# Performance work log

Measured on AMD Instinct MI355X. Metric: run time of the kernel, lower is better.

Reference implementation:

```python
import jax, jax.numpy as jnp
import numpy as np

D_MODEL = 4096
D_HIDDEN = 32768
BATCH = 2048
K = 128
N_DEAD = 2048


def _ln(x, eps=1e-5):
    # torch .std() is unbiased (ddof=1)
    mu = jnp.mean(x, axis=-1, keepdims=True)
    xc = x - mu
    std = jnp.std(x, axis=-1, keepdims=True, ddof=1)
    return xc / (std + eps), mu, std


def _topk_activation(x, k):
    # topk over last dim, relu values, scatter back into zeros
    vals, idx = jax.lax.top_k(x, k)          # [B, k]
    vals = jax.nn.relu(vals)
    rows = jnp.arange(x.shape[0])[:, None]    # [B, 1]
    return jnp.zeros_like(x).at[rows, idx].set(vals)


def setup_inputs() -> dict:
    key = jax.random.key(0)
    k1, k2 = jax.random.split(key)
    x = jax.random.normal(k1, (BATCH, D_MODEL), dtype=jnp.float32)
    # kaiming-uniform-ish encoder init
    bound = 1.0 / np.sqrt(D_MODEL)
    w_enc = jax.random.uniform(k2, (D_MODEL, D_HIDDEN), dtype=jnp.float32,
                               minval=-bound, maxval=bound)
    w_dec = w_enc.T
    w_dec = w_dec / jnp.linalg.norm(w_dec, axis=0, keepdims=True)
    b_enc = jnp.zeros((D_HIDDEN,), dtype=jnp.float32)
    b_pre = jnp.zeros((D_MODEL,), dtype=jnp.float32)
    # fixed dead-neuron mask with exactly N_DEAD dead latents
    dm = np.zeros((D_HIDDEN,), dtype=bool)
    rng = np.random.default_rng(0)
    dm[rng.choice(D_HIDDEN, size=N_DEAD, replace=False)] = True
    dead_mask = jnp.asarray(dm)
    return {"x": x, "w_enc": w_enc, "w_dec": w_dec, "b_enc": b_enc,
            "b_pre": b_pre, "dead_mask": dead_mask, "num_dead": N_DEAD}


def reference(x, w_enc, w_dec, b_enc, b_pre, dead_mask, num_dead):
    xn, mu, std = _ln(x)
    xc = xn - b_pre
    pre_acts = xc @ w_enc + b_enc                 # [B, d_hidden]
    latents = _topk_activation(pre_acts, K)
    recons = latents @ w_dec + b_pre              # [B, d_model]
    recons = recons * std + mu
    # auxk dead-neuron path (num_dead is a static python int)
    k_aux = min(x.shape[-1] // 2, num_dead)
    auxk_latents = jnp.where(dead_mask[None, :], pre_acts, -jnp.inf)
    auxk_acts = _topk_activation(auxk_latents, k_aux)
    auxk = auxk_acts @ w_dec + b_pre
    auxk = auxk * std + mu
    return recons, auxk, num_dead
```

## Files before the change

### kernel.cpp

```cpp
#include <hip/hip_runtime.h>
#include <math.h>

#define D_MODEL  4096
#define D_HIDDEN 32768
#define BATCH    2048
#define KSEL     128
#define NDEAD    2048
#define TIECAP   256

typedef short s16x8 __attribute__((ext_vector_type(8)));
typedef float f32x4 __attribute__((ext_vector_type(4)));

__device__ __forceinline__ unsigned int fkey(float f) {
    unsigned int u = __float_as_uint(f);
    return (u & 0x80000000u) ? ~u : (u | 0x80000000u);
}
__device__ __forceinline__ unsigned short f2bf(float f) {
    unsigned int u = __float_as_uint(f);
    u += 0x7FFFu + ((u >> 16) & 1u);
    return (unsigned short)(u >> 16);
}
__device__ __forceinline__ float bf2f(unsigned short h) {
    return __uint_as_float(((unsigned int)h) << 16);
}
__device__ __forceinline__ unsigned int key16x2(unsigned int u) {
    const unsigned int s = (u >> 15) & 0x10001u;
    const unsigned int mask = s * 0xFFFFu;
    return (u ^ mask) | (~mask & 0x80008000u);
}
__device__ __forceinline__ float unkey16(unsigned int k) {
    const unsigned int u = (k & 0x8000u) ? (k & 0x7FFFu) : (~k & 0xFFFFu);
    return __uint_as_float(u << 16);
}
__device__ __forceinline__ void async_copy16(void* lds_dst, const void* gsrc) {
    __builtin_amdgcn_global_load_lds(
        (const __attribute__((address_space(1))) unsigned int*)gsrc,
        (__attribute__((address_space(3))) unsigned int*)lds_dst,
        16, 0, 0);
}

__global__ __launch_bounds__(256) void prep_kernel(
    const float* __restrict__ x, const float* __restrict__ b_pre,
    double* __restrict__ mu, double* __restrict__ stdv, double* __restrict__ sinv,
    unsigned short* __restrict__ Ahp, float* __restrict__ xch, float* __restrict__ xcl)
{
    const int row = blockIdx.x;
    const int tid = threadIdx.x;
    const float* xr = x + (size_t)row * D_MODEL;
    float xv[16];
#pragma unroll
    for (int i = 0; i < 16; ++i) xv[i] = xr[tid + 256 * i];
    double s = 0.0;
#pragma unroll
    for (int i = 0; i < 16; ++i) s += (double)xv[i];
    __shared__ double red[4];
    __shared__ double sh_mu, sh_si;
    const int lane = tid & 63, wid = tid >> 6;
#pragma unroll
    for (int off = 32; off > 0; off >>= 1) s += __shfl_down(s, off, 64);
    if (lane == 0) red[wid] = s;
    __syncthreads();
    if (tid == 0) sh_mu = (red[0] + red[1] + red[2] + red[3]) / (double)D_MODEL;
    __syncthreads();
    const double m = sh_mu;
    double s2 = 0.0;
#pragma unroll
    for (int i = 0; i < 16; ++i) { double d = (double)xv[i] - m; s2 += d * d; }
#pragma unroll
    for (int off = 32; off > 0; off >>= 1) s2 += __shfl_down(s2, off, 64);
    __syncthreads();
    if (lane == 0) red[wid] = s2;
    __syncthreads();
    if (tid == 0) {
        double var = (red[0] + red[1] + red[2] + red[3]) / (double)(D_MODEL - 1);
        double sd = sqrt(var);
        mu[row] = m;
        stdv[row] = sd;
        const double si = 1.0 / (sd + 1e-5);
        sinv[row] = si;
        sh_si = si;
    }
    __syncthreads();
    const double si = sh_si;
#pragma unroll
    for (int i = 0; i < 4; ++i) {
        const int j = (i * 256 + tid) * 4;
        const float4 x4 = *(const float4*)(xr + j);
        const float4 bp = *(const float4*)(b_pre + j);
        float vf[4], hi[4], lo[4];
        const float xe[4] = {x4.x, x4.y, x4.z, x4.w};
        const float be[4] = {bp.x, bp.y, bp.z, bp.w};
#pragma unroll
        for (int e = 0; e < 4; ++e) {
            const double t = ((double)xe[e] - m) * si;
            vf[e] = (float)t - be[e];
            const double a = t - (double)be[e];
            hi[e] = (float)a;
            lo[e] = (float)(a - (double)hi[e]);
        }
        uint2 hw;
        hw.x = (unsigned)f2bf(vf[0]) | ((unsigned)f2bf(vf[1]) << 16);
        hw.y = (unsigned)f2bf(vf[2]) | ((unsigned)f2bf(vf[3]) << 16);
        *(uint2*)(Ahp + (size_t)row * D_MODEL + j) = hw;
        *(float4*)(xch + (size_t)row * D_MODEL + j) = make_float4(hi[0], hi[1], hi[2], hi[3]);
        *(float4*)(xcl + (size_t)row * D_MODEL + j) = make_float4(lo[0], lo[1], lo[2], lo[3]);
    }
}

__global__ void dead_scan_kernel(const unsigned char* __restrict__ mask8,
                                 int* __restrict__ dead_idx, int* __restrict__ dead_cnt,
                                 const int* __restrict__ num_dead_in, float* __restrict__ out_last)
{
    const int lane = threadIdx.x;
    int c = 0;
    for (int j = lane; j < D_HIDDEN; j += 64) c += (mask8[j] != 0);
#pragma unroll
    for (int off = 32; off > 0; off >>= 1) c += __shfl_down(c, off, 64);
    const int total_u8 = __shfl(c, 0, 64);
    const bool u8mode = (total_u8 == NDEAD);
    const int* mask32 = (const int*)mask8;
    int cnt = 0;
    for (int base = 0; base < D_HIDDEN; base += 64) {
        const int j = base + lane;
        const bool d = u8mode ? (mask8[j] != 0) : (mask32[j] != 0);
        const unsigned long long b = __ballot(d);
        const int pre = __popcll(b & ((1ull << lane) - 1ull));
        if (d && (cnt + pre) < NDEAD) dead_idx[cnt + pre] = j;
        cnt += __popcll(b);
    }
    const int cc = cnt > NDEAD ? NDEAD : cnt;
    if (lane == 0) {
        *dead_cnt = cc;
        *out_last = (float)(*num_dead_in);
    }
    for (int t = cc + lane; t < NDEAD; t += 64) dead_idx[t] = 0;
}

__global__ __launch_bounds__(256) void bsplit_kernel(
    const float* __restrict__ w_enc, unsigned short* __restrict__ Bhp)
{
    __shared__ float t[32][33];
    const int bk = blockIdx.x * 32;
    const int bn = blockIdx.y * 32;
    const int tid = threadIdx.x;
    const int lr = tid >> 3, lc4 = (tid & 7) * 4;
    const float4 v = *(const float4*)(w_enc + (size_t)(bk + lr) * D_HIDDEN + bn + lc4);
    t[lr][lc4 + 0] = v.x; t[lr][lc4 + 1] = v.y; t[lr][lc4 + 2] = v.z; t[lr][lc4 + 3] = v.w;
    __syncthreads();
    float o[4];
#pragma unroll
    for (int j = 0; j < 4; ++j) o[j] = t[lc4 + j][lr];
    uint2 hw;
    hw.x = (unsigned)f2bf(o[0]) | ((unsigned)f2bf(o[1]) << 16);
    hw.y = (unsigned)f2bf(o[2]) | ((unsigned)f2bf(o[3]) << 16);
    *(uint2*)(Bhp + (size_t)(bn + lr) * D_MODEL + bk + lc4) = hw;
}

__global__ __launch_bounds__(256) void wencT_kernel(
    const float* __restrict__ w_enc, float* __restrict__ wT)
{
    __shared__ float t[32][33];
    const int bk = blockIdx.x * 32;
    const int bn = blockIdx.y * 32;
    const int tid = threadIdx.x;
    const int lr = tid >> 3, lc4 = (tid & 7) * 4;
    const float4 v = *(const float4*)(w_enc + (size_t)(bk + lr) * D_HIDDEN + bn + lc4);
    t[lr][lc4 + 0] = v.x; t[lr][lc4 + 1] = v.y; t[lr][lc4 + 2] = v.z; t[lr][lc4 + 3] = v.w;
    __syncthreads();
    const int j = tid >> 3, i4 = (tid & 7) * 4;
    float4 o;
    o.x = t[i4 + 0][j]; o.y = t[i4 + 1][j]; o.z = t[i4 + 2][j]; o.w = t[i4 + 3][j];
    *(float4*)(wT + (size_t)(bn + j) * D_MODEL + bk + i4) = o;
}

__global__ __launch_bounds__(256) void wprep_kernel(
    const float* __restrict__ w_enc, unsigned short* __restrict__ Bhp,
    float* __restrict__ wT)
{
    __shared__ float t[32][33];
    const int bk = blockIdx.x * 32;
    const int bn = blockIdx.y * 32;
    const int tid = threadIdx.x;
    const int lr = tid >> 3, lc4 = (tid & 7) * 4;
    const float4 v = *(const float4*)(w_enc + (size_t)(bk + lr) * D_HIDDEN + bn + lc4);
    t[lr][lc4 + 0] = v.x; t[lr][lc4 + 1] = v.y; t[lr][lc4 + 2] = v.z; t[lr][lc4 + 3] = v.w;
    __syncthreads();
    float o[4];
#pragma unroll
    for (int j = 0; j < 4; ++j) o[j] = t[lc4 + j][lr];
    uint2 hw;
    hw.x = (unsigned)f2bf(o[0]) | ((unsigned)f2bf(o[1]) << 16);
    hw.y = (unsigned)f2bf(o[2]) | ((unsigned)f2bf(o[3]) << 16);
    *(uint2*)(Bhp + (size_t)(bn + lr) * D_MODEL + bk + lc4) = hw;
    *(float4*)(wT + (size_t)(bn + lr) * D_MODEL + bk + lc4) = make_float4(o[0], o[1], o[2], o[3]);
}

template<int EPI>
__global__ __launch_bounds__(512) void mm256_kernel(
    const unsigned short* __restrict__ A, const unsigned short* __restrict__ B,
    const int kdim, const int ntiles_x,
    const float* __restrict__ bias_n,
    const double* __restrict__ muv, const double* __restrict__ stdvv,
    void* __restrict__ outp, const long ostride)
{
    __shared__ unsigned short lds[2 * 4 * 8192];
    const int tid = threadIdx.x;
    const int lane = tid & 63, wid = tid >> 6;
    const int cpx = gridDim.x >> 3;
    const int orig = blockIdx.x;
    const int wg = (orig & 7) * cpx + (orig >> 3);
    const int m0 = (wg % ntiles_x) * 256;
    const int n0 = (wg / ntiles_x) * 256;
    const int wm = (wid >> 2) * 128;
    const int wn = (wid & 3) * 64;
    const int fr = lane & 15, kq = lane >> 4;
    const int swr = (fr >> 1) & 3;
    const int qg = (lane & 3) ^ ((lane >> 3) & 3);
    const int qo = (kq ^ swr) * 8;

    f32x4 acc[8][4];
#pragma unroll
    for (int i = 0; i < 8; ++i)
#pragma unroll
        for (int j = 0; j < 4; ++j) acc[i][j] = (f32x4){0.f, 0.f, 0.f, 0.f};

    const unsigned short* sH0[4];
    int dH0[4];
#pragma unroll
    for (int j = 0; j < 4; ++j) {
        const int g = wid * 4 + j;
        const int is_b = g >> 4;
        const int sr = g & 15;
        const unsigned short* gp = is_b ? B : A;
        const int t0 = is_b ? n0 : m0;
        sH0[j] = gp + (size_t)(t0 + sr * 16 + (lane >> 2)) * kdim + qg * 8;
        dH0[j] = (is_b ? 2 : 0) * 8192 + sr * 512;
    }

    const int NT = kdim >> 6;
#pragma unroll
    for (int j = 0; j < 4; ++j) async_copy16(lds + dH0[j], sH0[j]);
#pragma unroll
    for (int j = 0; j < 4; ++j) async_copy16(lds + 8192 + dH0[j], sH0[j] + 32);
    if (NT > 1) {
#pragma unroll
        for (int j = 0; j < 4; ++j) async_copy16(lds + 32768 + dH0[j], sH0[j] + 64);
    }

    for (int t = 0; t < NT; ++t) {
        const int cur = t & 1;
        unsigned short* bb = (unsigned short*)lds + cur * 32768;
        unsigned short* nb = (unsigned short*)lds + (cur ^ 1) * 32768;
        const int k1 = (t + 1) << 6;
        const int k2 = (t + 2) << 6;

        if (t < NT - 1) { asm volatile("s_waitcnt vmcnt(8)" ::: "memory"); }
        else            { asm volatile("s_waitcnt vmcnt(4)" ::: "memory"); }
        asm volatile("s_barrier" ::: "memory");
        __builtin_amdgcn_sched_barrier(0);
        {
            if (t + 1 < NT) {
                async_copy16(nb + 8192 + dH0[0], sH0[0] + k1 + 32);
                async_copy16(nb + 8192 + dH0[1], sH0[1] + k1 + 32);
            }
            s16x8 a[4], b[4];
#pragma unroll
            for (int mi = 0; mi < 4; ++mi)
                a[mi] = *(const s16x8*)(bb + (wm + mi * 16 + fr) * 32 + qo);
#pragma unroll
            for (int ni = 0; ni < 4; ++ni)
                b[ni] = *(const s16x8*)(bb + 2 * 8192 + (wn + ni * 16 + fr) * 32 + qo);
            __builtin_amdgcn_s_setprio(1);
#pragma unroll
            for (int mi = 0; mi < 4; ++mi)
#pragma unroll
                for (int ni = 0; ni < 4; ++ni)
                    acc[mi][ni] = __builtin_amdgcn_mfma_f32_16x16x32_bf16(a[mi], b[ni], acc[mi][ni], 0, 0, 0);
            __builtin_amdgcn_s_setprio(0);
            asm volatile("s_barrier" ::: "memory");
            __builtin_amdgcn_sched_barrier(0);
            if (t + 1 < NT) {
                async_copy16(nb + 8192 + dH0[2], sH0[2] + k1 + 32);
                async_copy16(nb + 8192 + dH0[3], sH0[3] + k1 + 32);
            }
            s16x8 a2[4];
#pragma unroll
            for (int mi = 0; mi < 4; ++mi)
                a2[mi] = *(const s16x8*)(bb + (wm + (mi + 4) * 16 + fr) * 32 + qo);
            __builtin_amdgcn_s_setprio(1);
#pragma unroll
            for (int mi = 0; mi < 4; ++mi)
#pragma unroll
                for (int ni = 0; ni < 4; ++ni)
                    acc[mi + 4][ni] = __builtin_amdgcn_mfma_f32_16x16x32_bf16(a2[mi], b[ni], acc[mi + 4][ni], 0, 0, 0);
            __builtin_amdgcn_s_setprio(0);
        }
        if (t < NT - 1) { asm volatile("s_waitcnt vmcnt(8)" ::: "memory"); }
        else            { asm volatile("s_waitcnt vmcnt(0)" ::: "memory"); }
        asm volatile("s_barrier" ::: "memory");
        __builtin_amdgcn_sched_barrier(0);
        {
            if (t + 2 < NT) {
                async_copy16(bb + dH0[0], sH0[0] + k2);
                async_copy16(bb + dH0[1], sH0[1] + k2);
            }
            s16x8 a[4], b[4];
#pragma unroll
            for (int mi = 0; mi < 4; ++mi)
                a[mi] = *(const s16x8*)(bb + 8192 + (wm + mi * 16 + fr) * 32 + qo);
#pragma unroll
            for (int ni = 0; ni < 4; ++ni)
                b[ni] = *(const s16x8*)(bb + 3 * 8192 + (wn + ni * 16 + fr) * 32 + qo);
            __builtin_amdgcn_s_setprio(1);
#pragma unroll
            for (int mi = 0; mi < 4; ++mi)
#pragma unroll
                for (int ni = 0; ni < 4; ++ni)
                    acc[mi][ni] = __builtin_amdgcn_mfma_f32_16x16x32_bf16(a[mi], b[ni], acc[mi][ni], 0, 0, 0);
            __builtin_amdgcn_s_setprio(0);
            asm volatile("s_barrier" ::: "memory");
            __builtin_amdgcn_sched_barrier(0);
            if (t + 2 < NT) {
                async_copy16(bb + dH0[2], sH0[2] + k2);
                async_copy16(bb + dH0[3], sH0[3] + k2);
            }
            s16x8 a2[4];
#pragma unroll
            for (int mi = 0; mi < 4; ++mi)
                a2[mi] = *(const s16x8*)(bb + 8192 + (wm + (mi + 4) * 16 + fr) * 32 + qo);
            __builtin_amdgcn_s_setprio(1);
#pragma unroll
            for (int mi = 0; mi < 4; ++mi)
#pragma unroll
                for (int ni = 0; ni < 4; ++ni)
                    acc[mi + 4][ni] = __builtin_amdgcn_mfma_f32_16x16x32_bf16(a2[mi], b[ni], acc[mi + 4][ni], 0, 0, 0);
            __builtin_amdgcn_s_setprio(0);
        }
    }

#pragma unroll
    for (int ni = 0; ni < 4; ++ni) {
        const int col = n0 + wn + ni * 16 + fr;
        const float be = bias_n[col];
#pragma unroll
        for (int mi = 0; mi < 8; ++mi) {
            const int rb = m0 + wm + mi * 16 + kq * 4;
            if (EPI == 0) {
                unsigned short* O = (unsigned short*)outp;
#pragma unroll
                for (int r = 0; r < 4; ++r)
                    O[(size_t)(rb + r) * ostride + col] = f2bf(acc[mi][ni][r] + be);
            } else {
                float* O = (float*)outp;
#pragma unroll
                for (int r = 0; r < 4; ++r) {
                    const int m = rb + r;
                    O[(size_t)m * ostride + col] =
                        (acc[mi][ni][r] + be) * (float)stdvv[m] + (float)muv[m];
                }
            }
        }
    }
}

template<int EPI>
__global__ __launch_bounds__(256) void mm_kernel(
    const unsigned short* __restrict__ A, const unsigned short* __restrict__ B,
    const int kdim, const int ntiles_x,
    const float* __restrict__ bias_n,
    const double* __restrict__ muv, const double* __restrict__ stdvv,
    void* __restrict__ outp, const long ostride)
{
    __shared__ unsigned short lds[3 * 2 * 128 * 32];
    const int tid = threadIdx.x;
    const int lane = tid & 63, wid = tid >> 6;
    const int cpx = gridDim.x >> 3;
    const int orig = blockIdx.x;
    const int wg = (orig & 7) * cpx + (orig >> 3);
    const int m0 = (wg % ntiles_x) * 128;
    const int n0 = (wg / ntiles_x) * 128;
    const int wm = (wid >> 1) * 64, wn = (wid & 1) * 64;
    const int fr = lane & 15, kq = lane >> 4;
    const int swr = (fr >> 1) & 3;
    const int qg = (lane & 3) ^ ((lane >> 3) & 3);
    const int qo = (kq ^ swr) * 8;

    f32x4 acc[4][4];
#pragma unroll
    for (int i = 0; i < 4; ++i)
#pragma unroll
        for (int j = 0; j < 4; ++j) acc[i][j] = (f32x4){0.f, 0.f, 0.f, 0.f};

    const unsigned short* srcs[4];
    int d0[4];
#pragma unroll
    for (int j = 0; j < 4; ++j) {
        const int s = wid * 4 + j;
        const int pl = s >> 3, sr = s & 7;
        const int r = sr * 16 + (lane >> 2);
        srcs[j] = (pl ? B : A) + (size_t)((pl ? n0 : m0) + r) * kdim + qg * 8;
        d0[j] = pl * 4096 + sr * 512;
    }

    const int NT = kdim >> 5;
#pragma unroll
    for (int j = 0; j < 4; ++j) async_copy16(lds + 0 * 8192 + d0[j], srcs[j]);
#pragma unroll
    for (int j = 0; j < 4; ++j) async_copy16(lds + 1 * 8192 + d0[j], srcs[j] + 32);

    int cur = 0, nxt = 2;
    for (int t = 0; t < NT; ++t) {
        if (t < NT - 1) {
            asm volatile("s_waitcnt vmcnt(4)" ::: "memory");
        } else {
            asm volatile("s_waitcnt vmcnt(0)" ::: "memory");
        }
        __builtin_amdgcn_s_barrier();
        __builtin_amdgcn_sched_barrier(0);

        if (t + 2 < NT) {
            const int k2 = (t + 2) << 5;
#pragma unroll
            for (int j = 0; j < 4; ++j) async_copy16(lds + nxt * 8192 + d0[j], srcs[j] + k2);
        }

        const unsigned short* la = lds + cur * 8192;
        const unsigned short* lb = la + 4096;
        s16x8 a[4], b[4];
#pragma unroll
        for (int i = 0; i < 4; ++i) {
            a[i] = *(const s16x8*)(la + (wm + i * 16 + fr) * 32 + qo);
            b[i] = *(const s16x8*)(lb + (wn + i * 16 + fr) * 32 + qo);
        }
#pragma unroll
        for (int mi = 0; mi < 4; ++mi)
#pragma unroll
            for (int ni = 0; ni < 4; ++ni)
                acc[mi][ni] = __builtin_amdgcn_mfma_f32_16x16x32_bf16(a[mi], b[ni], acc[mi][ni], 0, 0, 0);

        cur = cur == 2 ? 0 : cur + 1;
        nxt = nxt == 2 ? 0 : nxt + 1;
    }

#pragma unroll
    for (int ni = 0; ni < 4; ++ni) {
        const int col = n0 + wn + ni * 16 + fr;
        const float be = bias_n[col];
#pragma unroll
        for (int mi = 0; mi < 4; ++mi) {
            const int rb = m0 + wm + mi * 16 + kq * 4;
            if (EPI == 0) {
                unsigned short* O = (unsigned short*)outp;
#pragma unroll
                for (int r = 0; r < 4; ++r)
                    O[(size_t)(rb + r) * ostride + col] = f2bf(acc[mi][ni][r] + be);
            } else {
                float* O = (float*)outp;
#pragma unroll
                for (int r = 0; r < 4; ++r) {
                    const int m = rb + r;
                    O[(size_t)m * ostride + col] =
                        (acc[mi][ni][r] + be) * (float)stdvv[m] + (float)muv[m];
                }
            }
        }
    }
}

__global__ __launch_bounds__(256) void topk_sel_kernel(
    const unsigned short* __restrict__ p16,
    int* __restrict__ topk_idx, float* __restrict__ topk_val,
    int* __restrict__ sure_cnt, int* __restrict__ tie_cnt, int* __restrict__ cand_col)
{
    const int row = blockIdx.x;
    const int tid = threadIdx.x;
    const int lane = tid & 63, wid = tid >> 6;
    const unsigned short* pr = p16 + (size_t)row * D_HIDDEN;

    __shared__ int red[4];
    __shared__ int sh_sel, sh_tie;

    uint4 kr[16];
#pragma unroll
    for (int i = 0; i < 16; ++i) {
        uint4 w = *(const uint4*)(pr + (i * 256 + tid) * 8);
        w.x = key16x2(w.x); w.y = key16x2(w.y); w.z = key16x2(w.z); w.w = key16x2(w.w);
        kr[i] = w;
    }
    if (tid == 0) { sh_sel = 0; sh_tie = 0; }

    unsigned int lo = 0, hi = 65535;
    while (lo < hi) {
        const unsigned int mid = (lo + hi) >> 1;
        int c = 0;
#pragma unroll
        for (int i = 0; i < 16; ++i) {
            const unsigned int u[4] = {kr[i].x, kr[i].y, kr[i].z, kr[i].w};
#pragma unroll
            for (int e = 0; e < 4; ++e) {
                c += (int)((u[e] & 0xFFFFu) > mid);
                c += (int)((u[e] >> 16) > mid);
            }
        }
#pragma unroll
        for (int off = 32; off > 0; off >>= 1) c += __shfl_down(c, off, 64);
        if (lane == 0) red[wid] = c;
        __syncthreads();
        const int total = red[0] + red[1] + red[2] + red[3];
        if (total < KSEL) hi = mid; else lo = mid + 1;
        __syncthreads();
    }
    const unsigned int K16 = lo;

    const float vc = unkey16(K16);
    const float DLT = 1.3e-2f;
    const float sureT = vc + 2.f * DLT;
    const float candT = vc - 2.f * DLT;
    const unsigned int sK = fkey(sureT) >> 16;
    const unsigned int cK = fkey(candT) >> 16;

    int* oidx = topk_idx + row * KSEL;
    float* oval = topk_val + row * KSEL;
    int* cc = cand_col + row * TIECAP;
#pragma unroll
    for (int i = 0; i < 16; ++i) {
        const int j0 = (i * 256 + tid) * 8;
        const unsigned int u[4] = {kr[i].x, kr[i].y, kr[i].z, kr[i].w};
#pragma unroll
        for (int e = 0; e < 8; ++e) {
            const unsigned int k = (e & 1) ? (u[e >> 1] >> 16) : (u[e >> 1] & 0xFFFFu);
            if (k < cK) continue;
            const float v = unkey16(k);
            if (k > sK && v > sureT) {
                const int pos = atomicAdd(&sh_sel, 1);
                oidx[pos] = j0 + e;
                oval[pos] = v > 0.f ? v : 0.f;
            } else if (v >= candT) {
                const int t = atomicAdd(&sh_tie, 1);
                if (t < TIECAP) cc[t] = j0 + e;
            }
        }
    }
    __syncthreads();
    if (tid == 0) {
        sure_cnt[row] = sh_sel;
        tie_cnt[row] = sh_tie > TIECAP ? TIECAP : sh_tie;
    }
}

__global__ __launch_bounds__(256) void topk_refine_kernel(
    const int* __restrict__ tie_cnt, const int* __restrict__ cand_col,
    double* __restrict__ cand_val,
    const float* __restrict__ xch, const float* __restrict__ xcl,
    const float* __restrict__ wT, const float* __restrict__ b_enc)
{
    const int row = blockIdx.x;
    const int tid = threadIdx.x;
    const int lane = tid & 63, wid = tid >> 6;
    const int T = tie_cnt[row];
    const int base = (int)blockIdx.y * 4 + wid;
    if (base >= T) return;
    const float* hr = xch + (size_t)row * D_MODEL;
    const float* lr2 = xcl + (size_t)row * D_MODEL;
    for (int slot = base; slot < T; slot += 64) {
        const int col = cand_col[row * TIECAP + slot];
        const float* wr = wT + (size_t)col * D_MODEL;
        double s0 = 0.0, s1 = 0.0;
        for (int k = lane * 4; k < D_MODEL; k += 512) {
            {
                const float4 h = *(const float4*)(hr + k);
                const float4 l = *(const float4*)(lr2 + k);
                const float4 w4 = *(const float4*)(wr + k);
                s0 += ((double)h.x + (double)l.x) * (double)w4.x;
                s0 += ((double)h.y + (double)l.y) * (double)w4.y;
                s0 += ((double)h.z + (double)l.z) * (double)w4.z;
                s0 += ((double)h.w + (double)l.w) * (double)w4.w;
            }
            {
                const int k2 = k + 256;
                const float4 h = *(const float4*)(hr + k2);
                const float4 l = *(const float4*)(lr2 + k2);
                const float4 w4 = *(const float4*)(wr + k2);
                s1 += ((double)h.x + (double)l.x) * (double)w4.x;
                s1 += ((double)h.y + (double)l.y) * (double)w4.y;
                s1 += ((double)h.z + (double)l.z) * (double)w4.z;
                s1 += ((double)h.w + (double)l.w) * (double)w4.w;
            }
        }
        double s = s0 + s1;
#pragma unroll
        for (int off = 32; off > 0; off >>= 1) s += __shfl_down(s, off, 64);
        if (lane == 0) cand_val[row * TIECAP + slot] = s + (double)b_enc[col];
    }
}

__global__ __launch_bounds__(256) void topk_fin_kernel(
    const int* __restrict__ sure_cnt, const int* __restrict__ tie_cnt,
    const int* __restrict__ cand_col, const double* __restrict__ cand_val,
    int* __restrict__ topk_idx, float* __restrict__ topk_val)
{
    const int row = blockIdx.x;
    const int tid = threadIdx.x;
    __shared__ double vals[TIECAP];
    __shared__ int cols[TIECAP];
    const int G = sure_cnt[row];
    const int T = tie_cnt[row];
    const int R = KSEL - G;
    if (tid < T) {
        vals[tid] = cand_val[row * TIECAP + tid];
        cols[tid] = cand_col[row * TIECAP + tid];
    }
    __syncthreads();
    int* oidx = topk_idx + row * KSEL;
    float* oval = topk_val + row * KSEL;
    if (tid < T) {
        const double v = vals[tid];
        const int c = cols[tid];
        int rank = 0;
        for (int u = 0; u < T; ++u) {
            const double vu = vals[u];
            rank += (int)((vu > v) || (vu == v && cols[u] < c));
        }
        if (rank < R) {
            oidx[G + rank] = c;
            oval[G + rank] = v > 0.0 ? (float)v : 0.f;
        }
    }
    const int take = R < T ? R : T;
    if (tid >= take && tid < R) {
        oidx[G + tid] = (T > 0) ? cols[0] : 0;
        oval[G + tid] = 0.f;
    }
}

__global__ __launch_bounds__(256) void wdec2bf_kernel(
    const float* __restrict__ w_dec, unsigned short* __restrict__ wd16)
{
    const size_t gid = (size_t)blockIdx.x * 256 + threadIdx.x;
    const size_t base = gid * 8;
    const float4 a = *(const float4*)(w_dec + base);
    const float4 b = *(const float4*)(w_dec + base + 4);
    uint4 o;
    o.x = (unsigned)f2bf(a.x) | ((unsigned)f2bf(a.y) << 16);
    o.y = (unsigned)f2bf(a.z) | ((unsigned)f2bf(a.w) << 16);
    o.z = (unsigned)f2bf(b.x) | ((unsigned)f2bf(b.y) << 16);
    o.w = (unsigned)f2bf(b.z) | ((unsigned)f2bf(b.w) << 16);
    *(uint4*)(wd16 + base) = o;
}

__global__ __launch_bounds__(256) void decode_kernel(
    const int* __restrict__ topk_idx, const float* __restrict__ topk_val,
    const unsigned short* __restrict__ wd16, const float* __restrict__ b_pre,
    const double* __restrict__ mu, const double* __restrict__ stdv,
    float* __restrict__ out0)
{
    const int row = blockIdx.x;
    const int tid = threadIdx.x;
    __shared__ int sidx[KSEL];
    __shared__ float sval[KSEL];
    if (tid < KSEL) {
        sidx[tid] = topk_idx[row * KSEL + tid];
        sval[tid] = topk_val[row * KSEL + tid];
    }
    __syncthreads();
    float acc[16];
#pragma unroll
    for (int i = 0; i < 16; ++i) acc[i] = 0.f;
    const int dbase = tid * 16;
    for (int k = 0; k < KSEL; ++k) {
        const float v = sval[k];
        if (v == 0.f) continue;
        const uint4* wr = (const uint4*)(wd16 + (size_t)sidx[k] * D_MODEL + dbase);
        const uint4 w0 = wr[0], w1 = wr[1];
        const unsigned int u[8] = {w0.x, w0.y, w0.z, w0.w, w1.x, w1.y, w1.z, w1.w};
#pragma unroll
        for (int i = 0; i < 8; ++i) {
            acc[2 * i]     += v * __uint_as_float(u[i] << 16);
            acc[2 * i + 1] += v * __uint_as_float(u[i] & 0xFFFF0000u);
        }
    }
    const float st = (float)stdv[row];
    const float mm = (float)mu[row];
    float* o = out0 + (size_t)row * D_MODEL + dbase;
#pragma unroll
    for (int i = 0; i < 16; ++i) {
        o[i] = (acc[i] + b_pre[dbase + i]) * st + mm;
    }
}

__global__ __launch_bounds__(256) void auxg_kernel(
    const unsigned short* __restrict__ p16, const int* __restrict__ dead_idx,
    const int* __restrict__ dead_cnt, unsigned short* __restrict__ Ahd)
{
    const int r = blockIdx.x;
    const int tid = threadIdx.x;
    const int dc = *dead_cnt;
#pragma unroll
    for (int i = 0; i < 8; ++i) {
        const int c = i * 256 + tid;
        unsigned short v = 0;
        if (c < dc) {
            const unsigned short u = p16[(size_t)r * D_HIDDEN + dead_idx[c]];
            v = (u & 0x8000u) ? (unsigned short)0 : u;
        }
        Ahd[(size_t)r * NDEAD + c] = v;
    }
}

__global__ __launch_bounds__(256) void auxb_kernel(
    const float* __restrict__ w_dec, const int* __restrict__ dead_idx,
    unsigned short* __restrict__ Bhd)
{
    __shared__ float t[32][33];
    const int k0 = blockIdx.x * 32;
    const int n0 = blockIdx.y * 32;
    const int tid = threadIdx.x;
    const int i = tid >> 3, j4 = (tid & 7) * 4;
    const int srow = dead_idx[k0 + i];
    const float4 v = *(const float4*)(w_dec + (size_t)srow * D_MODEL + n0 + j4);
    t[i][j4 + 0] = v.x; t[i][j4 + 1] = v.y; t[i][j4 + 2] = v.z; t[i][j4 + 3] = v.w;
    __syncthreads();
    const int j = tid >> 3, i4 = (tid & 7) * 4;
    uint2 hw;
    hw.x = (unsigned)f2bf(t[i4 + 0][j]) | ((unsigned)f2bf(t[i4 + 1][j]) << 16);
    hw.y = (unsigned)f2bf(t[i4 + 2][j]) | ((unsigned)f2bf(t[i4 + 3][j]) << 16);
    *(uint2*)(Bhd + (size_t)(n0 + j) * NDEAD + k0 + i4) = hw;
}

extern "C" void kernel_launch(void* const* d_in, const int* in_sizes, int n_in,
                              void* d_out, int out_size, void* d_ws, size_t ws_size,
                              hipStream_t stream)
{
    (void)in_sizes; (void)n_in; (void)out_size;
    const float* x      = (const float*)d_in[0];
    const float* w_enc  = (const float*)d_in[1];
    const float* w_dec  = (const float*)d_in[2];
    const float* b_enc  = (const float*)d_in[3];
    const float* b_pre  = (const float*)d_in[4];
    const unsigned char* dead_mask = (const unsigned char*)d_in[5];
    const int* num_dead = (const int*)d_in[6];
    float* out = (float*)d_out;

    char* base = (char*)d_ws;
    char* w = base;
    auto alloc = [&](size_t bytes) -> char* {
        char* p = w;
        w += (bytes + 255) & ~(size_t)255;
        return p;
    };
    unsigned short* p16 = (unsigned short*)alloc((size_t)BATCH * D_HIDDEN * 2);
    double* mu       = (double*)alloc((size_t)BATCH * 8);
    double* stdv     = (double*)alloc((size_t)BATCH * 8);
    double* sinv     = (double*)alloc((size_t)BATCH * 8);
    int* topk_idx    = (int*)alloc((size_t)BATCH * KSEL * 4);
    float* topk_val  = (float*)alloc((size_t)BATCH * KSEL * 4);
    int* dead_idx    = (int*)alloc((size_t)NDEAD * 4);
    int* dead_cnt    = (int*)alloc(256);
    int* sure_cnt    = (int*)alloc((size_t)BATCH * 4);
    int* tie_cnt     = (int*)alloc((size_t)BATCH * 4);
    int* cand_col    = (int*)alloc((size_t)BATCH * TIECAP * 4);
    double* cand_val = (double*)alloc((size_t)BATCH * TIECAP * 8);
    float* xch       = (float*)alloc((size_t)BATCH * D_MODEL * 4);
    float* xcl       = (float*)alloc((size_t)BATCH * D_MODEL * 4);
    unsigned short* Ahp = (unsigned short*)alloc((size_t)BATCH * D_MODEL * 2);
    char* region     = alloc((size_t)D_HIDDEN * D_MODEL * 4);
    const size_t need_small = (size_t)(w - base);
    float* wT_big    = (float*)alloc((size_t)D_HIDDEN * D_MODEL * 4);
    const size_t need_big = (size_t)(w - base);
    const bool bigws = (ws_size >= need_big);
    (void)need_small;

    unsigned short* Bhp = (unsigned short*)region;
    float* wT_small = (float*)region;
    unsigned short* wd16 = (unsigned short*)region;
    unsigned short* Bhd  = (unsigned short*)(region + (size_t)D_HIDDEN * D_MODEL * 2);
    unsigned short* Ahd  = Ahp;
    float* wT = bigws ? wT_big : wT_small;

    float* out0 = out;
    float* out1 = out + (size_t)BATCH * D_MODEL;
    float* out_last = out + (size_t)2 * BATCH * D_MODEL;

    prep_kernel<<<BATCH, 256, 0, stream>>>(x, b_pre, mu, stdv, sinv, Ahp, xch, xcl);
    dead_scan_kernel<<<1, 64, 0, stream>>>(dead_mask, dead_idx, dead_cnt, num_dead, out_last);
    if (bigws) {
        wprep_kernel<<<dim3(D_MODEL / 32, D_HIDDEN / 32), 256, 0, stream>>>(w_enc, Bhp, wT);
    } else {
        bsplit_kernel<<<dim3(D_MODEL / 32, D_HIDDEN / 32), 256, 0, stream>>>(w_enc, Bhp);
    }
    mm256_kernel<0><<<(BATCH / 256) * (D_HIDDEN / 256), 512, 0, stream>>>(
        Ahp, Bhp, D_MODEL, BATCH / 256, b_enc, nullptr, nullptr, p16, (long)D_HIDDEN);
    if (!bigws) {
        wencT_kernel<<<dim3(D_MODEL / 32, D_HIDDEN / 32), 256, 0, stream>>>(w_enc, wT);
    }
    topk_sel_kernel<<<BATCH, 256, 0, stream>>>(p16, topk_idx, topk_val, sure_cnt, tie_cnt, cand_col);
    topk_refine_kernel<<<dim3(BATCH, 16), 256, 0, stream>>>(
        tie_cnt, cand_col, cand_val, xch, xcl, wT, b_enc);
    topk_fin_kernel<<<BATCH, 256, 0, stream>>>(
        sure_cnt, tie_cnt, cand_col, cand_val, topk_idx, topk_val);
    auxg_kernel<<<BATCH, 256, 0, stream>>>(p16, dead_idx, dead_cnt, Ahd);
    auxb_kernel<<<dim3(NDEAD / 32, D_MODEL / 32), 256, 0, stream>>>(w_dec, dead_idx, Bhd);
    wdec2bf_kernel<<<(int)(((size_t)D_HIDDEN * D_MODEL) / (256 * 8)), 256, 0, stream>>>(w_dec, wd16);
    decode_kernel<<<BATCH, 256, 0, stream>>>(topk_idx, topk_val, wd16, b_pre, mu, stdv, out0);
    mm_kernel<1><<<(BATCH / 128) * (D_MODEL / 128), 256, 0, stream>>>(
        Ahd, Bhd, NDEAD, BATCH / 128, b_pre, mu, stdv, out1, (long)D_MODEL);
}
```

Before: 2.123 ms.

## Merge small kernels into combined launches and reuse 256-tile GEMM for aux path

Folds the dead-mask scan into an extra block of the prep kernel, and merges top-k selection, aux gather, aux weight transpose and decoder bf16 conversion into one block-partitioned kernel. It also merges top-k finalization into the decode kernel, keeping the selected indices in shared memory. The aux GEMM now uses the 256-tile mm256 kernel instead of the 128-tile one. This cuts launch count and lets independent work share the GPU at once, at the cost of a heterogeneous grid whose blocks differ in register and LDS use.

```diff
diff --git a/kernel.cpp b/kernel.cpp
--- a/kernel.cpp
+++ b/kernel.cpp
@@ -8,6 +8,11 @@
 #define NDEAD    2048
 #define TIECAP   256
 
+#define NB_SEL 2048
+#define NB_AG  2048
+#define NB_AB  8192
+#define NB_WD  8192
+
 typedef short s16x8 __attribute__((ext_vector_type(8)));
 typedef float f32x4 __attribute__((ext_vector_type(4)));
 
@@ -42,10 +47,40 @@
 __global__ __launch_bounds__(256) void prep_kernel(
     const float* __restrict__ x, const float* __restrict__ b_pre,
     double* __restrict__ mu, double* __restrict__ stdv, double* __restrict__ sinv,
-    unsigned short* __restrict__ Ahp, float* __restrict__ xch, float* __restrict__ xcl)
+    unsigned short* __restrict__ Ahp, float* __restrict__ xch, float* __restrict__ xcl,
+    const unsigned char* __restrict__ mask8, int* __restrict__ dead_idx,
+    int* __restrict__ dead_cnt, const int* __restrict__ num_dead_in,
+    float* __restrict__ out_last)
 {
     const int row = blockIdx.x;
     const int tid = threadIdx.x;
+    if (row == BATCH) {
+        if (tid >= 64) return;
+        const int lane = tid;
+        int c = 0;
+        for (int j = lane; j < D_HIDDEN; j += 64) c += (mask8[j] != 0);
+#pragma unroll
+        for (int off = 32; off > 0; off >>= 1) c += __shfl_down(c, off, 64);
+        const int total_u8 = __shfl(c, 0, 64);
+        const bool u8mode = (total_u8 == NDEAD);
+        const int* mask32 = (const int*)mask8;
+        int cnt = 0;
+        for (int base = 0; base < D_HIDDEN; base += 64) {
+            const int j = base + lane;
+            const bool d = u8mode ? (mask8[j] != 0) : (mask32[j] != 0);
+            const unsigned long long b = __ballot(d);
+            const int pre = __popcll(b & ((1ull << lane) - 1ull));
+            if (d && (cnt + pre) < NDEAD) dead_idx[cnt + pre] = j;
+            cnt += __popcll(b);
+        }
+        const int cc = cnt > NDEAD ? NDEAD : cnt;
+        if (lane == 0) {
+            *dead_cnt = cc;
+            *out_last = (float)(*num_dead_in);
+        }
+        for (int t = cc + lane; t < NDEAD; t += 64) dead_idx[t] = 0;
+        return;
+    }
     const float* xr = x + (size_t)row * D_MODEL;
     float xv[16];
 #pragma unroll
@@ -105,35 +140,6 @@
         *(float4*)(xch + (size_t)row * D_MODEL + j) = make_float4(hi[0], hi[1], hi[2], hi[3]);
         *(float4*)(xcl + (size_t)row * D_MODEL + j) = make_float4(lo[0], lo[1], lo[2], lo[3]);
     }
-}
-
-__global__ void dead_scan_kernel(const unsigned char* __restrict__ mask8,
-                                 int* __restrict__ dead_idx, int* __restrict__ dead_cnt,
-                                 const int* __restrict__ num_dead_in, float* __restrict__ out_last)
-{
-    const int lane = threadIdx.x;
-    int c = 0;
-    for (int j = lane; j < D_HIDDEN; j += 64) c += (mask8[j] != 0);
-#pragma unroll
-    for (int off = 32; off > 0; off >>= 1) c += __shfl_down(c, off, 64);
-    const int total_u8 = __shfl(c, 0, 64);
-    const bool u8mode = (total_u8 == NDEAD);
-    const int* mask32 = (const int*)mask8;
-    int cnt = 0;
-    for (int base = 0; base < D_HIDDEN; base += 64) {
-        const int j = base + lane;
-        const bool d = u8mode ? (mask8[j] != 0) : (mask32[j] != 0);
-        const unsigned long long b = __ballot(d);
-        const int pre = __popcll(b & ((1ull << lane) - 1ull));
-        if (d && (cnt + pre) < NDEAD) dead_idx[cnt + pre] = j;
-        cnt += __popcll(b);
-    }
-    const int cc = cnt > NDEAD ? NDEAD : cnt;
-    if (lane == 0) {
-        *dead_cnt = cc;
-        *out_last = (float)(*num_dead_in);
-    }
-    for (int t = cc + lane; t < NDEAD; t += 64) dead_idx[t] = 0;
 }
 
 __global__ __launch_bounds__(256) void bsplit_kernel(
@@ -363,189 +369,175 @@
     }
 }
 
-template<int EPI>
-__global__ __launch_bounds__(256) void mm_kernel(
-    const unsigned short* __restrict__ A, const unsigned short* __restrict__ B,
-    const int kdim, const int ntiles_x,
-    const float* __restrict__ bias_n,
-    const double* __restrict__ muv, const double* __restrict__ stdvv,
-    void* __restrict__ outp, const long ostride)
-{
-    __shared__ unsigned short lds[3 * 2 * 128 * 32];
-    const int tid = threadIdx.x;
-    const int lane = tid & 63, wid = tid >> 6;
-    const int cpx = gridDim.x >> 3;
-    const int orig = blockIdx.x;
-    const int wg = (orig & 7) * cpx + (orig >> 3);
-    const int m0 = (wg % ntiles_x) * 128;
-    const int n0 = (wg / ntiles_x) * 128;
-    const int wm = (wid >> 1) * 64, wn = (wid & 1) * 64;
-    const int fr = lane & 15, kq = lane >> 4;
-    const int swr = (fr >> 1) & 3;
-    const int qg = (lane & 3) ^ ((lane >> 3) & 3);
-    const int qo = (kq ^ swr) * 8;
-
-    f32x4 acc[4][4];
-#pragma unroll
-    for (int i = 0; i < 4; ++i)
-#pragma unroll
-        for (int j = 0; j < 4; ++j) acc[i][j] = (f32x4){0.f, 0.f, 0.f, 0.f};
-
-    const unsigned short* srcs[4];
-    int d0[4];
-#pragma unroll
-    for (int j = 0; j < 4; ++j) {
-        const int s = wid * 4 + j;
-        const int pl = s >> 3, sr = s & 7;
-        const int r = sr * 16 + (lane >> 2);
-        srcs[j] = (pl ? B : A) + (size_t)((pl ? n0 : m0) + r) * kdim + qg * 8;
-        d0[j] = pl * 4096 + sr * 512;
-    }
-
-    const int NT = kdim >> 5;
-#pragma unroll
-    for (int j = 0; j < 4; ++j) async_copy16(lds + 0 * 8192 + d0[j], srcs[j]);
-#pragma unroll
-    for (int j = 0; j < 4; ++j) async_copy16(lds + 1 * 8192 + d0[j], srcs[j] + 32);
-
-    int cur = 0, nxt = 2;
-    for (int t = 0; t < NT; ++t) {
-        if (t < NT - 1) {
-            asm volatile("s_waitcnt vmcnt(4)" ::: "memory");
-        } else {
-            asm volatile("s_waitcnt vmcnt(0)" ::: "memory");
-        }
-        __builtin_amdgcn_s_barrier();
-        __builtin_amdgcn_sched_barrier(0);
-
-        if (t + 2 < NT) {
-            const int k2 = (t + 2) << 5;
-#pragma unroll
-            for (int j = 0; j < 4; ++j) async_copy16(lds + nxt * 8192 + d0[j], srcs[j] + k2);
-        }
-
-        const unsigned short* la = lds + cur * 8192;
-        const unsigned short* lb = la + 4096;
-        s16x8 a[4], b[4];
-#pragma unroll
-        for (int i = 0; i < 4; ++i) {
-            a[i] = *(const s16x8*)(la + (wm + i * 16 + fr) * 32 + qo);
-            b[i] = *(const s16x8*)(lb + (wn + i * 16 + fr) * 32 + qo);
-        }
-#pragma unroll
-        for (int mi = 0; mi < 4; ++mi)
-#pragma unroll
-            for (int ni = 0; ni < 4; ++ni)
-                acc[mi][ni] = __builtin_amdgcn_mfma_f32_16x16x32_bf16(a[mi], b[ni], acc[mi][ni], 0, 0, 0);
-
-        cur = cur == 2 ? 0 : cur + 1;
-        nxt = nxt == 2 ? 0 : nxt + 1;
-    }
-
-#pragma unroll
-    for (int ni = 0; ni < 4; ++ni) {
-        const int col = n0 + wn + ni * 16 + fr;
-        const float be = bias_n[col];
-#pragma unroll
-        for (int mi = 0; mi < 4; ++mi) {
-            const int rb = m0 + wm + mi * 16 + kq * 4;
-            if (EPI == 0) {
-                unsigned short* O = (unsigned short*)outp;
-#pragma unroll
-                for (int r = 0; r < 4; ++r)
-                    O[(size_t)(rb + r) * ostride + col] = f2bf(acc[mi][ni][r] + be);
-            } else {
-                float* O = (float*)outp;
-#pragma unroll
-                for (int r = 0; r < 4; ++r) {
-                    const int m = rb + r;
-                    O[(size_t)m * ostride + col] =
-                        (acc[mi][ni][r] + be) * (float)stdvv[m] + (float)muv[m];
-                }
-            }
-        }
-    }
-}
-
-__global__ __launch_bounds__(256) void topk_sel_kernel(
+__global__ __launch_bounds__(256) void comboA_kernel(
     const unsigned short* __restrict__ p16,
     int* __restrict__ topk_idx, float* __restrict__ topk_val,
-    int* __restrict__ sure_cnt, int* __restrict__ tie_cnt, int* __restrict__ cand_col)
-{
-    const int row = blockIdx.x;
-    const int tid = threadIdx.x;
-    const int lane = tid & 63, wid = tid >> 6;
-    const unsigned short* pr = p16 + (size_t)row * D_HIDDEN;
-
+    int* __restrict__ sure_cnt, int* __restrict__ tie_cnt, int* __restrict__ cand_col,
+    const int* __restrict__ dead_idx, const int* __restrict__ dead_cnt,
+    unsigned short* __restrict__ Ahd,
+    const float* __restrict__ w_dec, unsigned short* __restrict__ Bhd,
+    unsigned short* __restrict__ wd16,
+    const int nb_ab, const int nb_wd)
+{
+    const int b = blockIdx.x;
+    const int tid = threadIdx.x;
+    __shared__ float tsm[32][33];
     __shared__ int red[4];
     __shared__ int sh_sel, sh_tie;
 
-    uint4 kr[16];
-#pragma unroll
-    for (int i = 0; i < 16; ++i) {
-        uint4 w = *(const uint4*)(pr + (i * 256 + tid) * 8);
-        w.x = key16x2(w.x); w.y = key16x2(w.y); w.z = key16x2(w.z); w.w = key16x2(w.w);
-        kr[i] = w;
-    }
-    if (tid == 0) { sh_sel = 0; sh_tie = 0; }
-
-    unsigned int lo = 0, hi = 65535;
-    while (lo < hi) {
-        const unsigned int mid = (lo + hi) >> 1;
-        int c = 0;
+    if (b < NB_SEL) {
+        const int row = b;
+        const int lane = tid & 63, wid = tid >> 6;
+        const unsigned short* pr = p16 + (size_t)row * D_HIDDEN;
+        uint4 kr[16];
 #pragma unroll
         for (int i = 0; i < 16; ++i) {
+            uint4 w = *(const uint4*)(pr + (i * 256 + tid) * 8);
+            w.x = key16x2(w.x); w.y = key16x2(w.y); w.z = key16x2(w.z); w.w = key16x2(w.w);
+            kr[i] = w;
+        }
+        if (tid == 0) { sh_sel = 0; sh_tie = 0; }
+        unsigned int lo = 0, hi = 65535;
+        while (lo < hi) {
+            const unsigned int mid = (lo + hi) >> 1;
+            int c = 0;
+#pragma unroll
+            for (int i = 0; i < 16; ++i) {
+                const unsigned int u[4] = {kr[i].x, kr[i].y, kr[i].z, kr[i].w};
+#pragma unroll
+                for (int e = 0; e < 4; ++e) {
+                    c += (int)((u[e] & 0xFFFFu) > mid);
+                    c += (int)((u[e] >> 16) > mid);
+                }
+            }
+#pragma unroll
+            for (int off = 32; off > 0; off >>= 1) c += __shfl_down(c, off, 64);
+            if (lane == 0) red[wid] = c;
+            __syncthreads();
+            const int total = red[0] + red[1] + red[2] + red[3];
+            if (total < KSEL) hi = mid; else lo = mid + 1;
+            __syncthreads();
+        }
+        const unsigned int K16 = lo;
+        const float vc = unkey16(K16);
+        const float DLT = 1.3e-2f;
+        const float sureT = vc + 2.f * DLT;
+        const float candT = vc - 2.f * DLT;
+        const unsigned int sK = fkey(sureT) >> 16;
+        const unsigned int cK = fkey(candT) >> 16;
+        int* oidx = topk_idx + row * KSEL;
+        float* oval = topk_val + row * KSEL;
+        int* cc = cand_col + row * TIECAP;
+#pragma unroll
+        for (int i = 0; i < 16; ++i) {
+            const int j0 = (i * 256 + tid) * 8;
             const unsigned int u[4] = {kr[i].x, kr[i].y, kr[i].z, kr[i].w};
 #pragma unroll
-            for (int e = 0; e < 4; ++e) {
-                c += (int)((u[e] & 0xFFFFu) > mid);
-                c += (int)((u[e] >> 16) > mid);
-            }
-        }
-#pragma unroll
-        for (int off = 32; off > 0; off >>= 1) c += __shfl_down(c, off, 64);
-        if (lane == 0) red[wid] = c;
+            for (int e = 0; e < 8; ++e) {
+                const unsigned int k = (e & 1) ? (u[e >> 1] >> 16) : (u[e >> 1] & 0xFFFFu);
+                if (k < cK) continue;
+                const float v = unkey16(k);
+                if (k > sK && v > sureT) {
+                    const int pos = atomicAdd(&sh_sel, 1);
+                    oidx[pos] = j0 + e;
+                    oval[pos] = v > 0.f ? v : 0.f;
+                } else if (v >= candT) {
+                    const int t = atomicAdd(&sh_tie, 1);
+                    if (t < TIECAP) cc[t] = j0 + e;
+                }
+            }
+        }
         __syncthreads();
-        const int total = red[0] + red[1] + red[2] + red[3];
-        if (total < KSEL) hi = mid; else lo = mid + 1;
+        if (tid == 0) {
+            sure_cnt[row] = sh_sel;
+            tie_cnt[row] = sh_tie > TIECAP ? TIECAP : sh_tie;
+        }
+        return;
+    }
+    if (b < NB_SEL + NB_AG) {
+        const int r = b - NB_SEL;
+        const int dc = *dead_cnt;
+#pragma unroll
+        for (int i = 0; i < 8; ++i) {
+            const int c = i * 256 + tid;
+            unsigned short v = 0;
+            if (c < dc) {
+                const unsigned short u = p16[(size_t)r * D_HIDDEN + dead_idx[c]];
+                v = (u & 0x8000u) ? (unsigned short)0 : u;
+            }
+            Ahd[(size_t)r * NDEAD + c] = v;
+        }
+        return;
+    }
+    if (b < NB_SEL + NB_AG + nb_ab) {
+        const int idx = b - (NB_SEL + NB_AG);
+        const int k0 = (idx & 63) * 32;
+        const int n0 = (idx >> 6) * 32;
+        const int i = tid >> 3, j4 = (tid & 7) * 4;
+        const int srow = dead_idx[k0 + i];
+        const float4 v = *(const float4*)(w_dec + (size_t)srow * D_MODEL + n0 + j4);
+        tsm[i][j4 + 0] = v.x; tsm[i][j4 + 1] = v.y; tsm[i][j4 + 2] = v.z; tsm[i][j4 + 3] = v.w;
         __syncthreads();
-    }
-    const unsigned int K16 = lo;
-
-    const float vc = unkey16(K16);
-    const float DLT = 1.3e-2f;
-    const float sureT = vc + 2.f * DLT;
-    const float candT = vc - 2.f * DLT;
-    const unsigned int sK = fkey(sureT) >> 16;
-    const unsigned int cK = fkey(candT) >> 16;
-
-    int* oidx = topk_idx + row * KSEL;
-    float* oval = topk_val + row * KSEL;
-    int* cc = cand_col + row * TIECAP;
-#pragma unroll
-    for (int i = 0; i < 16; ++i) {
-        const int j0 = (i * 256 + tid) * 8;
-        const unsigned int u[4] = {kr[i].x, kr[i].y, kr[i].z, kr[i].w};
-#pragma unroll
-        for (int e = 0; e < 8; ++e) {
-            const unsigned int k = (e & 1) ? (u[e >> 1] >> 16) : (u[e >> 1] & 0xFFFFu);
-            if (k < cK) continue;
-            const float v = unkey16(k);
-            if (k > sK && v > sureT) {
-                const int pos = atomicAdd(&sh_sel, 1);
-                oidx[pos] = j0 + e;
-                oval[pos] = v > 0.f ? v : 0.f;
-            } else if (v >= candT) {
-                const int t = atomicAdd(&sh_tie, 1);
-                if (t < TIECAP) cc[t] = j0 + e;
-            }
-        }
-    }
-    __syncthreads();
-    if (tid == 0) {
-        sure_cnt[row] = sh_sel;
-        tie_cnt[row] = sh_tie > TIECAP ? TIECAP : sh_tie;
-    }
+        const int j = tid >> 3, i4 = (tid & 7) * 4;
+        uint2 hw;
+        hw.x = (unsigned)f2bf(tsm[i4 + 0][j]) | ((unsigned)f2bf(tsm[i4 + 1][j]) << 16);
+        hw.y = (unsigned)f2bf(tsm[i4 + 2][j]) | ((unsigned)f2bf(tsm[i4 + 3][j]) << 16);
+        *(uint2*)(Bhd + (size_t)(n0 + j) * NDEAD + k0 + i4) = hw;
+        return;
+    }
+    {
+        const int bb = b - (NB_SEL + NB_AG + nb_ab);
+        (void)nb_wd;
+        const size_t base0 = (size_t)bb * 16384;
+#pragma unroll
+        for (int it = 0; it < 8; ++it) {
+            const size_t off = base0 + (size_t)it * 2048 + (size_t)tid * 8;
+            const float4 a = *(const float4*)(w_dec + off);
+            const float4 c = *(const float4*)(w_dec + off + 4);
+            uint4 o;
+            o.x = (unsigned)f2bf(a.x) | ((unsigned)f2bf(a.y) << 16);
+            o.y = (unsigned)f2bf(a.z) | ((unsigned)f2bf(a.w) << 16);
+            o.z = (unsigned)f2bf(c.x) | ((unsigned)f2bf(c.y) << 16);
+            o.w = (unsigned)f2bf(c.z) | ((unsigned)f2bf(c.w) << 16);
+            *(uint4*)(wd16 + off) = o;
+        }
+        return;
+    }
+}
+
+__global__ __launch_bounds__(256) void auxb_kernel(
+    const float* __restrict__ w_dec, const int* __restrict__ dead_idx,
+    unsigned short* __restrict__ Bhd)
+{
+    __shared__ float t[32][33];
+    const int k0 = blockIdx.x * 32;
+    const int n0 = blockIdx.y * 32;
+    const int tid = threadIdx.x;
+    const int i = tid >> 3, j4 = (tid & 7) * 4;
+    const int srow = dead_idx[k0 + i];
+    const float4 v = *(const float4*)(w_dec + (size_t)srow * D_MODEL + n0 + j4);
+    t[i][j4 + 0] = v.x; t[i][j4 + 1] = v.y; t[i][j4 + 2] = v.z; t[i][j4 + 3] = v.w;
+    __syncthreads();
+    const int j = tid >> 3, i4 = (tid & 7) * 4;
+    uint2 hw;
+    hw.x = (unsigned)f2bf(t[i4 + 0][j]) | ((unsigned)f2bf(t[i4 + 1][j]) << 16);
+    hw.y = (unsigned)f2bf(t[i4 + 2][j]) | ((unsigned)f2bf(t[i4 + 3][j]) << 16);
+    *(uint2*)(Bhd + (size_t)(n0 + j) * NDEAD + k0 + i4) = hw;
+}
+
+__global__ __launch_bounds__(256) void wdec2bf_kernel(
+    const float* __restrict__ w_dec, unsigned short* __restrict__ wd16)
+{
+    const size_t gid = (size_t)blockIdx.x * 256 + threadIdx.x;
+    const size_t base = gid * 8;
+    const float4 a = *(const float4*)(w_dec + base);
+    const float4 b = *(const float4*)(w_dec + base + 4);
+    uint4 o;
+    o.x = (unsigned)f2bf(a.x) | ((unsigned)f2bf(a.y) << 16);
+    o.y = (unsigned)f2bf(a.z) | ((unsigned)f2bf(a.w) << 16);
+    o.z = (unsigned)f2bf(b.x) | ((unsigned)f2bf(b.y) << 16);
+    o.w = (unsigned)f2bf(b.z) | ((unsigned)f2bf(b.w) << 16);
+    *(uint4*)(wd16 + base) = o;
 }
 
 __global__ __launch_bounds__(256) void topk_refine_kernel(
@@ -594,15 +586,20 @@
     }
 }
 
-__global__ __launch_bounds__(256) void topk_fin_kernel(
+__global__ __launch_bounds__(256) void decode_fin_kernel(
     const int* __restrict__ sure_cnt, const int* __restrict__ tie_cnt,
     const int* __restrict__ cand_col, const double* __restrict__ cand_val,
-    int* __restrict__ topk_idx, float* __restrict__ topk_val)
+    const int* __restrict__ topk_idx, const float* __restrict__ topk_val,
+    const unsigned short* __restrict__ wd16, const float* __restrict__ b_pre,
+    const double* __restrict__ mu, const double* __restrict__ stdv,
+    float* __restrict__ out0)
 {
     const int row = blockIdx.x;
     const int tid = threadIdx.x;
     __shared__ double vals[TIECAP];
     __shared__ int cols[TIECAP];
+    __shared__ int sidx[KSEL];
+    __shared__ float sval[KSEL];
     const int G = sure_cnt[row];
     const int T = tie_cnt[row];
     const int R = KSEL - G;
@@ -610,9 +607,11 @@
         vals[tid] = cand_val[row * TIECAP + tid];
         cols[tid] = cand_col[row * TIECAP + tid];
     }
-    __syncthreads();
-    int* oidx = topk_idx + row * KSEL;
-    float* oval = topk_val + row * KSEL;
+    if (tid < G) {
+        sidx[tid] = topk_idx[row * KSEL + tid];
+        sval[tid] = topk_val[row * KSEL + tid];
+    }
+    __syncthreads();
     if (tid < T) {
         const double v = vals[tid];
         const int c = cols[tid];
@@ -622,45 +621,14 @@
             rank += (int)((vu > v) || (vu == v && cols[u] < c));
         }
         if (rank < R) {
-            oidx[G + rank] = c;
-            oval[G + rank] = v > 0.0 ? (float)v : 0.f;
+            sidx[G + rank] = c;
+            sval[G + rank] = v > 0.0 ? (float)v : 0.f;
         }
     }
     const int take = R < T ? R : T;
     if (tid >= take && tid < R) {
-        oidx[G + tid] = (T > 0) ? cols[0] : 0;
-        oval[G + tid] = 0.f;
-    }
-}
-
-__global__ __launch_bounds__(256) void wdec2bf_kernel(
-    const float* __restrict__ w_dec, unsigned short* __restrict__ wd16)
-{
-    const size_t gid = (size_t)blockIdx.x * 256 + threadIdx.x;
-    const size_t base = gid * 8;
-    const float4 a = *(const float4*)(w_dec + base);
-    const float4 b = *(const float4*)(w_dec + base + 4);
-    uint4 o;
-    o.x = (unsigned)f2bf(a.x) | ((unsigned)f2bf(a.y) << 16);
-    o.y = (unsigned)f2bf(a.z) | ((unsigned)f2bf(a.w) << 16);
-    o.z = (unsigned)f2bf(b.x) | ((unsigned)f2bf(b.y) << 16);
-    o.w = (unsigned)f2bf(b.z) | ((unsigned)f2bf(b.w) << 16);
-    *(uint4*)(wd16 + base) = o;
-}
-
-__global__ __launch_bounds__(256) void decode_kernel(
-    const int* __restrict__ topk_idx, const float* __restrict__ topk_val,
-    const unsigned short* __restrict__ wd16, const float* __restrict__ b_pre,
-    const double* __restrict__ mu, const double* __restrict__ stdv,
-    float* __restrict__ out0)
-{
-    const int row = blockIdx.x;
-    const int tid = threadIdx.x;
-    __shared__ int sidx[KSEL];
-    __shared__ float sval[KSEL];
-    if (tid < KSEL) {
-        sidx[tid] = topk_idx[row * KSEL + tid];
-        sval[tid] = topk_val[row * KSEL + tid];
+        sidx[G + tid] = (T > 0) ? cols[0] : 0;
+        sval[G + tid] = 0.f;
     }
     __syncthreads();
     float acc[16];
@@ -686,45 +654,6 @@
     for (int i = 0; i < 16; ++i) {
         o[i] = (acc[i] + b_pre[dbase + i]) * st + mm;
     }
-}
-
-__global__ __launch_bounds__(256) void auxg_kernel(
-    const unsigned short* __restrict__ p16, const int* __restrict__ dead_idx,
-    const int* __restrict__ dead_cnt, unsigned short* __restrict__ Ahd)
-{
-    const int r = blockIdx.x;
-    const int tid = threadIdx.x;
-    const int dc = *dead_cnt;
-#pragma unroll
-    for (int i = 0; i < 8; ++i) {
-        const int c = i * 256 + tid;
-        unsigned short v = 0;
-        if (c < dc) {
-            const unsigned short u = p16[(size_t)r * D_HIDDEN + dead_idx[c]];
-            v = (u & 0x8000u) ? (unsigned short)0 : u;
-        }
-        Ahd[(size_t)r * NDEAD + c] = v;
-    }
-}
-
-__global__ __launch_bounds__(256) void auxb_kernel(
-    const float* __restrict__ w_dec, const int* __restrict__ dead_idx,
-    unsigned short* __restrict__ Bhd)
-{
-    __shared__ float t[32][33];
-    const int k0 = blockIdx.x * 32;
-    const int n0 = blockIdx.y * 32;
-    const int tid = threadIdx.x;
-    const int i = tid >> 3, j4 = (tid & 7) * 4;
-    const int srow = dead_idx[k0 + i];
-    const float4 v = *(const float4*)(w_dec + (size_t)srow * D_MODEL + n0 + j4);
-    t[i][j4 + 0] = v.x; t[i][j4 + 1] = v.y; t[i][j4 + 2] = v.z; t[i][j4 + 3] = v.w;
-    __syncthreads();
-    const int j = tid >> 3, i4 = (tid & 7) * 4;
-    uint2 hw;
-    hw.x = (unsigned)f2bf(t[i4 + 0][j]) | ((unsigned)f2bf(t[i4 + 1][j]) << 16);
-    hw.y = (unsigned)f2bf(t[i4 + 2][j]) | ((unsigned)f2bf(t[i4 + 3][j]) << 16);
-    *(uint2*)(Bhd + (size_t)(n0 + j) * NDEAD + k0 + i4) = hw;
 }
 
 extern "C" void kernel_launch(void* const* d_in, const int* in_sizes, int n_in,
@@ -764,11 +693,9 @@
     float* xcl       = (float*)alloc((size_t)BATCH * D_MODEL * 4);
     unsigned short* Ahp = (unsigned short*)alloc((size_t)BATCH * D_MODEL * 2);
     char* region     = alloc((size_t)D_HIDDEN * D_MODEL * 4);
-    const size_t need_small = (size_t)(w - base);
     float* wT_big    = (float*)alloc((size_t)D_HIDDEN * D_MODEL * 4);
     const size_t need_big = (size_t)(w - base);
     const bool bigws = (ws_size >= need_big);
-    (void)need_small;
 
     unsigned short* Bhp = (unsigned short*)region;
     float* wT_small = (float*)region;
@@ -781,8 +708,8 @@
     float* out1 = out + (size_t)BATCH * D_MODEL;
     float* out_last = out + (size_t)2 * BATCH * D_MODEL;
 
-    prep_kernel<<<BATCH, 256, 0, stream>>>(x, b_pre, mu, stdv, sinv, Ahp, xch, xcl);
-    dead_scan_kernel<<<1, 64, 0, stream>>>(dead_mask, dead_idx, dead_cnt, num_dead, out_last);
+    prep_kernel<<<BATCH + 1, 256, 0, stream>>>(x, b_pre, mu, stdv, sinv, Ahp, xch, xcl,
+                                               dead_mask, dead_idx, dead_cnt, num_dead, out_last);
     if (bigws) {
         wprep_kernel<<<dim3(D_MODEL / 32, D_HIDDEN / 32), 256, 0, stream>>>(w_enc, Bhp, wT);
     } else {
@@ -790,18 +717,27 @@
     }
     mm256_kernel<0><<<(BATCH / 256) * (D_HIDDEN / 256), 512, 0, stream>>>(
         Ahp, Bhp, D_MODEL, BATCH / 256, b_enc, nullptr, nullptr, p16, (long)D_HIDDEN);
-    if (!bigws) {
+    if (bigws) {
+        comboA_kernel<<<NB_SEL + NB_AG + NB_AB + NB_WD, 256, 0, stream>>>(
+            p16, topk_idx, topk_val, sure_cnt, tie_cnt, cand_col,
+            dead_idx, dead_cnt, Ahd, w_dec, Bhd, wd16, NB_AB, NB_WD);
+        mm256_kernel<1><<<(BATCH / 256) * (D_MODEL / 256), 512, 0, stream>>>(
+            Ahd, Bhd, NDEAD, BATCH / 256, b_pre, mu, stdv, out1, (long)D_MODEL);
+        topk_refine_kernel<<<dim3(BATCH, 16), 256, 0, stream>>>(
+            tie_cnt, cand_col, cand_val, xch, xcl, wT, b_enc);
+    } else {
         wencT_kernel<<<dim3(D_MODEL / 32, D_HIDDEN / 32), 256, 0, stream>>>(w_enc, wT);
-    }
-    topk_sel_kernel<<<BATCH, 256, 0, stream>>>(p16, topk_idx, topk_val, sure_cnt, tie_cnt, cand_col);
-    topk_refine_kernel<<<dim3(BATCH, 16), 256, 0, stream>>>(
-        tie_cnt, cand_col, cand_val, xch, xcl, wT, b_enc);
-    topk_fin_kernel<<<BATCH, 256, 0, stream>>>(
-        sure_cnt, tie_cnt, cand_col, cand_val, topk_idx, topk_val);
-    auxg_kernel<<<BATCH, 256, 0, stream>>>(p16, dead_idx, dead_cnt, Ahd);
-    auxb_kernel<<<dim3(NDEAD / 32, D_MODEL / 32), 256, 0, stream>>>(w_dec, dead_idx, Bhd);
-    wdec2bf_kernel<<<(int)(((size_t)D_HIDDEN * D_MODEL) / (256 * 8)), 256, 0, stream>>>(w_dec, wd16);
-    decode_kernel<<<BATCH, 256, 0, stream>>>(topk_idx, topk_val, wd16, b_pre, mu, stdv, out0);
-    mm_kernel<1><<<(BATCH / 128) * (D_MODEL / 128), 256, 0, stream>>>(
-        Ahd, Bhd, NDEAD, BATCH / 128, b_pre, mu, stdv, out1, (long)D_MODEL);
-}
+        comboA_kernel<<<NB_SEL + NB_AG, 256, 0, stream>>>(
+            p16, topk_idx, topk_val, sure_cnt, tie_cnt, cand_col,
+            dead_idx, dead_cnt, Ahd, w_dec, Bhd, wd16, 0, 0);
+        topk_refine_kernel<<<dim3(BATCH, 16), 256, 0, stream>>>(
+            tie_cnt, cand_col, cand_val, xch, xcl, wT, b_enc);
+        auxb_kernel<<<dim3(NDEAD / 32, D_MODEL / 32), 256, 0, stream>>>(w_dec, dead_idx, Bhd);
+        wdec2bf_kernel<<<(int)(((size_t)D_HIDDEN * D_MODEL) / (256 * 8)), 256, 0, stream>>>(w_dec, wd16);
+        mm256_kernel<1><<<(BATCH / 256) * (D_MODEL / 256), 512, 0, stream>>>(
+            Ahd, Bhd, NDEAD, BATCH / 256, b_pre, mu, stdv, out1, (long)D_MODEL);
+    }
+    decode_fin_kernel<<<BATCH, 256, 0, stream>>>(
+        sure_cnt, tie_cnt, cand_col, cand_val, topk_idx, topk_val,
+        wd16, b_pre, mu, stdv, out0);
+}
```

Result: faster. 2.069 ms (-2.6%).
